# Performance work log

Measured on AMD Instinct MI355X. Metric: run time of the kernel, lower is better.

## Reference

```python
import jax, jax.numpy as jnp
import numpy as np

B, D, H = 8192, 256, 512


def setup_inputs() -> dict:
    key = jax.random.key(0)
    ks = jax.random.split(key, 25)
    inp = {
        "x": jax.random.normal(ks[0], (B, D), jnp.float32),
        "h_t": jax.random.normal(ks[1], (B, H), jnp.float32),
        "h_s": jax.random.normal(ks[2], (B, H), jnp.float32),
        "c_t": jax.random.normal(ks[3], (B, H), jnp.float32),
        "c_s": jax.random.normal(ks[4], (B, H), jnp.float32),
    }
    names = ["Ui", "Wti", "Wsi", "bi", "Us", "Wts", "Wss", "bs",
             "Ut", "Wtt", "Wst", "bt", "Uo", "Wto", "Wso", "bo",
             "Uc", "Wtc", "Wsc", "bc"]
    shapes = {"U": (D, H), "W": (H, H), "b": (H,)}
    scale = 0.02  # keep activations in a sane range
    for i, n in enumerate(names):
        s = shapes["U"] if n[0] == "U" else (shapes["b"] if n[0] == "b" else shapes["W"])
        inp[n] = jax.random.normal(ks[5 + i], s, jnp.float32) * scale
    return inp


def reference(x, h_t, h_s, c_t, c_s,
              Ui, Wti, Wsi, bi, Us, Wts, Wss, bs,
              Ut, Wtt, Wst, bt, Uo, Wto, Wso, bo,
              Uc, Wtc, Wsc, bc):
    # Fuse the 15 small GEMMs into 3 concatenated GEMMs: [B,D]@[D,5H] etc.
    U = jnp.concatenate([Ui, Us, Ut, Uo, Uc], axis=1)      # [D, 5H]
    Wt = jnp.concatenate([Wti, Wts, Wtt, Wto, Wtc], axis=1)  # [H, 5H]
    Ws = jnp.concatenate([Wsi, Wss, Wst, Wso, Wsc], axis=1)  # [H, 5H]
    b = jnp.concatenate([bi, bs, bt, bo, bc])                # [5H]
    gates = x @ U + h_t @ Wt + h_s @ Ws + b                  # [B, 5H]
    g_i, g_fs, g_ft, g_o, g_c = jnp.split(gates, 5, axis=1)
    i_n = jax.nn.sigmoid(g_i)
    f_s_n = jax.nn.sigmoid(g_fs)
    f_t_n = jax.nn.sigmoid(g_ft)
    o_n = jax.nn.sigmoid(g_o)
    c_n = jnp.tanh(g_c)
    c_h = i_n * c_n + f_t_n * c_t + f_s_n * c_s
    h = o_n * jnp.tanh(c_h)
    return (h, c_h)
```

## Files before the change

### kernel.cpp

```cpp
#include <hip/hip_runtime.h>
#include <hip/hip_bf16.h>
#include <cstdint>
#include <cstddef>

#define B_  8192
#define D_  256
#define H_  512
#define K_  1280
#define N_  2560
#define NT_ 160

typedef short short8 __attribute__((ext_vector_type(8)));
typedef float f32x4  __attribute__((ext_vector_type(4)));

__device__ __forceinline__ float sigf(float x)     { return 1.f / (1.f + __expf(-x)); }
__device__ __forceinline__ float tanhfast(float x) { return 1.f - 2.f / (__expf(2.f * x) + 1.f); }

__global__ void convA_kernel(const float* __restrict__ x, const float* __restrict__ ht,
                             const float* __restrict__ hs, __hip_bfloat16* __restrict__ A) {
    int t = blockIdx.x * 256 + threadIdx.x;
    int idx8 = t * 8;
    int b = idx8 / K_;
    int k = idx8 - b * K_;
    const float* src;
    if (k < D_)            src = x  + (size_t)b * D_ + k;
    else if (k < D_ + H_)  src = ht + (size_t)b * H_ + (k - D_);
    else                   src = hs + (size_t)b * H_ + (k - D_ - H_);
    f32x4 v0 = *(const f32x4*)(src);
    f32x4 v1 = *(const f32x4*)(src + 4);
    union { short8 s; __hip_bfloat16 h[8]; } o;
    o.h[0] = __float2bfloat16(v0[0]); o.h[1] = __float2bfloat16(v0[1]);
    o.h[2] = __float2bfloat16(v0[2]); o.h[3] = __float2bfloat16(v0[3]);
    o.h[4] = __float2bfloat16(v1[0]); o.h[5] = __float2bfloat16(v1[1]);
    o.h[6] = __float2bfloat16(v1[2]); o.h[7] = __float2bfloat16(v1[3]);
    *(short8*)(A + idx8) = o.s;
}

struct WPtrs {
    const float* U[5];
    const float* Wt[5];
    const float* Ws[5];
};

__global__ void convW_kernel(WPtrs p, __hip_bfloat16* __restrict__ WT) {
    __shared__ __hip_bfloat16 tile[64][72];
    int g  = blockIdx.z;
    int k0 = blockIdx.y * 64;
    int h0 = blockIdx.x * 64;
    const float* src; int kl0;
    if (k0 < 256)      { src = p.U[g];  kl0 = k0; }
    else if (k0 < 768) { src = p.Wt[g]; kl0 = k0 - 256; }
    else               { src = p.Ws[g]; kl0 = k0 - 768; }
    int tid = threadIdx.x;
    int tk = tid >> 6;
    int th = tid & 63;
    for (int r = 0; r < 16; ++r) {
        int kl = r * 4 + tk;
        tile[kl][th] = __float2bfloat16(src[(size_t)(kl0 + kl) * H_ + h0 + th]);
    }
    __syncthreads();
    for (int r = 0; r < 16; ++r) {
        int hl = r * 4 + tk;
        int h  = h0 + hl;
        int np = (h >> 4) * 80 + g * 16 + (h & 15);
        WT[(size_t)np * K_ + k0 + th] = tile[th][hl];
    }
}

#define GLD16(gp, lp)                                                              \
    __builtin_amdgcn_global_load_lds(                                              \
        (const __attribute__((address_space(1))) unsigned int*)(gp),               \
        (__attribute__((address_space(3))) unsigned int*)(lp), 16, 0, 0)

__global__ __launch_bounds__(256) void gemm_fused_kernel(
    const __hip_bfloat16* __restrict__ A, const __hip_bfloat16* __restrict__ WT,
    const float* __restrict__ ct, const float* __restrict__ cs,
    const float* __restrict__ bi, const float* __restrict__ bfs,
    const float* __restrict__ bft, const float* __restrict__ bo,
    const float* __restrict__ bc, float* __restrict__ out) {
    __shared__ alignas(16) unsigned short sA[128 * 32];
    __shared__ alignas(16) unsigned short sB[NT_ * 32];

    int tid = threadIdx.x;
    int m0 = blockIdx.x * 128;
    int n0 = blockIdx.y * NT_;
    int wid  = tid >> 6, lane = tid & 63;
    int wm   = wid >> 1, wn   = wid & 1;
    int quad = lane >> 4, l15 = lane & 15;

    int h = (blockIdx.y * 2 + wn) * 16 + l15;
    float Bi = bi[h], Bfs = bfs[h], Bft = bft[h], Bo = bo[h], Bc = bc[h];

    f32x4 acc[4][5];
    for (int i = 0; i < 4; ++i)
        for (int j = 0; j < 5; ++j)
            acc[i][j] = (f32x4){0.f, 0.f, 0.f, 0.f};

    int srow = tid >> 2;
    int scol = (tid & 3) * 8;
    const __hip_bfloat16* Abase = A  + (size_t)(m0 + srow) * K_ + scol;
    const __hip_bfloat16* Bbase = WT + (size_t)(n0 + srow) * K_ + scol;
    unsigned short* AsDst = sA + tid * 8;
    unsigned short* BsDst = sB + tid * 8;

    for (int k0 = 0; k0 < K_; k0 += 32) {
        GLD16(Abase + k0,                    AsDst);
        GLD16(Abase + k0 + (size_t)64 * K_,  AsDst + 2048);
        GLD16(Bbase + k0,                    BsDst);
        GLD16(Bbase + k0 + (size_t)64 * K_,  BsDst + 2048);
        if (tid < 128)
            GLD16(Bbase + k0 + (size_t)128 * K_, BsDst + 4096);
        __syncthreads();

        short8 a[4];
        for (int f = 0; f < 4; ++f)
            a[f] = *(const short8*)(sA + (wm * 64 + f * 16 + l15) * 32 + quad * 8);
        for (int j = 0; j < 5; ++j) {
            short8 b = *(const short8*)(sB + (wn * 80 + j * 16 + l15) * 32 + quad * 8);
            for (int i = 0; i < 4; ++i)
                acc[i][j] = __builtin_amdgcn_mfma_f32_16x16x32_bf16(a[i], b, acc[i][j], 0, 0, 0);
        }
        __syncthreads();
    }

    for (int i = 0; i < 4; ++i) {
        int row0 = m0 + wm * 64 + i * 16 + quad * 4;
        for (int r = 0; r < 4; ++r) {
            size_t idx = (size_t)(row0 + r) * H_ + h;
            float i_n  = sigf(acc[i][0][r] + Bi);
            float fs_n = sigf(acc[i][1][r] + Bfs);
            float ft_n = sigf(acc[i][2][r] + Bft);
            float o_n  = sigf(acc[i][3][r] + Bo);
            float c_n  = tanhfast(acc[i][4][r] + Bc);
            float ch   = i_n * c_n + ft_n * ct[idx] + fs_n * cs[idx];
            out[idx] = o_n * tanhfast(ch);
            out[(size_t)B_ * H_ + idx] = ch;
        }
    }
}

struct AllW {
    const float* U[5];
    const float* Wt[5];
    const float* Ws[5];
    const float* bias[5];
};

__global__ __launch_bounds__(512) void fallback_kernel(const float* __restrict__ x,
                                                       const float* __restrict__ ht,
                                                       const float* __restrict__ hs,
                                                       const float* __restrict__ ct,
                                                       const float* __restrict__ cs,
                                                       AllW w, float* __restrict__ out) {
    __shared__ float arow[K_];
    int b = blockIdx.x;
    int h = threadIdx.x;
    for (int k = h; k < K_; k += 512) {
        float v;
        if (k < D_)           v = x[b * D_ + k];
        else if (k < D_ + H_) v = ht[b * H_ + k - D_];
        else                  v = hs[b * H_ + k - D_ - H_];
        arow[k] = v;
    }
    __syncthreads();
    float g[5];
    for (int gi = 0; gi < 5; ++gi) {
        float s = w.bias[gi][h];
        const float* U = w.U[gi];
        for (int k = 0; k < D_; ++k) s += arow[k] * U[(size_t)k * H_ + h];
        const float* Wt = w.Wt[gi];
        for (int k = 0; k < H_; ++k) s += arow[D_ + k] * Wt[(size_t)k * H_ + h];
        const float* Ws = w.Ws[gi];
        for (int k = 0; k < H_; ++k) s += arow[D_ + H_ + k] * Ws[(size_t)k * H_ + h];
        g[gi] = s;
    }
    int idx = b * H_ + h;
    float i_n = sigf(g[0]), fs_n = sigf(g[1]), ft_n = sigf(g[2]), o_n = sigf(g[3]);
    float c_n = tanhfast(g[4]);
    float ch  = i_n * c_n + ft_n * ct[idx] + fs_n * cs[idx];
    out[idx] = o_n * tanhfast(ch);
    out[(size_t)B_ * H_ + idx] = ch;
}

extern "C" void kernel_launch(void* const* d_in, const int* in_sizes, int n_in,
                              void* d_out, int out_size, void* d_ws, size_t ws_size,
                              hipStream_t stream) {
    const float* x  = (const float*)d_in[0];
    const float* ht = (const float*)d_in[1];
    const float* hs = (const float*)d_in[2];
    const float* ct = (const float*)d_in[3];
    const float* cs = (const float*)d_in[4];

    WPtrs wp;
    AllW  aw;
    const float* bias[5];
    for (int g = 0; g < 5; ++g) {
        wp.U[g]  = (const float*)d_in[5 + g * 4 + 0];
        wp.Wt[g] = (const float*)d_in[5 + g * 4 + 1];
        wp.Ws[g] = (const float*)d_in[5 + g * 4 + 2];
        bias[g]  = (const float*)d_in[5 + g * 4 + 3];
        aw.U[g] = wp.U[g]; aw.Wt[g] = wp.Wt[g]; aw.Ws[g] = wp.Ws[g]; aw.bias[g] = bias[g];
    }
    float* out = (float*)d_out;

    size_t szA = (size_t)B_ * K_ * 2;
    size_t szW = (size_t)N_ * K_ * 2;

    if (ws_size >= szA + szW) {
        __hip_bfloat16* Abf = (__hip_bfloat16*)d_ws;
        __hip_bfloat16* WT  = (__hip_bfloat16*)((char*)d_ws + szA);

        convA_kernel<<<(B_ * K_ / 8) / 256, 256, 0, stream>>>(x, ht, hs, Abf);
        convW_kernel<<<dim3(8, 20, 5), 256, 0, stream>>>(wp, WT);
        gemm_fused_kernel<<<dim3(B_ / 128, N_ / NT_), 256, 0, stream>>>(
            Abf, WT, ct, cs, bias[0], bias[1], bias[2], bias[3], bias[4], out);
    } else {
        fallback_kernel<<<B_, 512, 0, stream>>>(x, ht, hs, ct, cs, aw, out);
    }
}
```

Measured before the change: 245.0 us.

## Load GEMM operands directly from global into registers with software prefetch

Drops the LDS staging and both per-iteration barriers in the fused GEMM. Each wave now reads its A and B MFMA fragments straight from global memory into registers, double-buffered so the next K-slice loads while the current one computes. Launch bounds now request 3 blocks per CU. The cost is that fragments LDS used to share across the two waves with the same rows or columns are now fetched twice from global/L2. Each lane also reads only 16 bytes per row, which may leave loads poorly coalesced and raise register pressure.

```diff
diff --git a/kernel.cpp b/kernel.cpp
--- a/kernel.cpp
+++ b/kernel.cpp
@@ -67,20 +67,12 @@
     }
 }
 
-#define GLD16(gp, lp)                                                              \
-    __builtin_amdgcn_global_load_lds(                                              \
-        (const __attribute__((address_space(1))) unsigned int*)(gp),               \
-        (__attribute__((address_space(3))) unsigned int*)(lp), 16, 0, 0)
-
-__global__ __launch_bounds__(256) void gemm_fused_kernel(
+__global__ __launch_bounds__(256, 3) void gemm_fused_kernel(
     const __hip_bfloat16* __restrict__ A, const __hip_bfloat16* __restrict__ WT,
     const float* __restrict__ ct, const float* __restrict__ cs,
     const float* __restrict__ bi, const float* __restrict__ bfs,
     const float* __restrict__ bft, const float* __restrict__ bo,
     const float* __restrict__ bc, float* __restrict__ out) {
-    __shared__ alignas(16) unsigned short sA[128 * 32];
-    __shared__ alignas(16) unsigned short sB[NT_ * 32];
-
     int tid = threadIdx.x;
     int m0 = blockIdx.x * 128;
     int n0 = blockIdx.y * NT_;
@@ -92,39 +84,46 @@
     float Bi = bi[h], Bfs = bfs[h], Bft = bft[h], Bo = bo[h], Bc = bc[h];
 
     f32x4 acc[4][5];
+#pragma unroll
     for (int i = 0; i < 4; ++i)
+#pragma unroll
         for (int j = 0; j < 5; ++j)
             acc[i][j] = (f32x4){0.f, 0.f, 0.f, 0.f};
 
-    int srow = tid >> 2;
-    int scol = (tid & 3) * 8;
-    const __hip_bfloat16* Abase = A  + (size_t)(m0 + srow) * K_ + scol;
-    const __hip_bfloat16* Bbase = WT + (size_t)(n0 + srow) * K_ + scol;
-    unsigned short* AsDst = sA + tid * 8;
-    unsigned short* BsDst = sB + tid * 8;
-
-    for (int k0 = 0; k0 < K_; k0 += 32) {
-        GLD16(Abase + k0,                    AsDst);
-        GLD16(Abase + k0 + (size_t)64 * K_,  AsDst + 2048);
-        GLD16(Bbase + k0,                    BsDst);
-        GLD16(Bbase + k0 + (size_t)64 * K_,  BsDst + 2048);
-        if (tid < 128)
-            GLD16(Bbase + k0 + (size_t)128 * K_, BsDst + 4096);
-        __syncthreads();
-
-        short8 a[4];
-        for (int f = 0; f < 4; ++f)
-            a[f] = *(const short8*)(sA + (wm * 64 + f * 16 + l15) * 32 + quad * 8);
-        for (int j = 0; j < 5; ++j) {
-            short8 b = *(const short8*)(sB + (wn * 80 + j * 16 + l15) * 32 + quad * 8);
+    const __hip_bfloat16* aRow = A  + (size_t)(m0 + wm * 64 + l15) * K_ + quad * 8;
+    const __hip_bfloat16* bRow = WT + (size_t)(n0 + wn * 80 + l15) * K_ + quad * 8;
+
+    short8 ca[4], cb[5], na[4], nb[5];
+#pragma unroll
+    for (int f = 0; f < 4; ++f) ca[f] = *(const short8*)(aRow + (size_t)f * 16 * K_);
+#pragma unroll
+    for (int j = 0; j < 5; ++j) cb[j] = *(const short8*)(bRow + (size_t)j * 16 * K_);
+
+    for (int kk = 32; kk < K_; kk += 32) {
+#pragma unroll
+        for (int f = 0; f < 4; ++f) na[f] = *(const short8*)(aRow + (size_t)f * 16 * K_ + kk);
+#pragma unroll
+        for (int j = 0; j < 5; ++j) nb[j] = *(const short8*)(bRow + (size_t)j * 16 * K_ + kk);
+#pragma unroll
+        for (int j = 0; j < 5; ++j)
+#pragma unroll
             for (int i = 0; i < 4; ++i)
-                acc[i][j] = __builtin_amdgcn_mfma_f32_16x16x32_bf16(a[i], b, acc[i][j], 0, 0, 0);
-        }
-        __syncthreads();
-    }
-
+                acc[i][j] = __builtin_amdgcn_mfma_f32_16x16x32_bf16(ca[i], cb[j], acc[i][j], 0, 0, 0);
+#pragma unroll
+        for (int f = 0; f < 4; ++f) ca[f] = na[f];
+#pragma unroll
+        for (int j = 0; j < 5; ++j) cb[j] = nb[j];
+    }
+#pragma unroll
+    for (int j = 0; j < 5; ++j)
+#pragma unroll
+        for (int i = 0; i < 4; ++i)
+            acc[i][j] = __builtin_amdgcn_mfma_f32_16x16x32_bf16(ca[i], cb[j], acc[i][j], 0, 0, 0);
+
+#pragma unroll
     for (int i = 0; i < 4; ++i) {
         int row0 = m0 + wm * 64 + i * 16 + quad * 4;
+#pragma unroll
         for (int r = 0; r < 4; ++r) {
             size_t idx = (size_t)(row0 + r) * H_ + h;
             float i_n  = sigf(acc[i][0][r] + Bi);
```

Result: slower. 341.3 us (+39.3%).
